# Kernel tuning notes

Measured on AMD Instinct MI355X. Metric: run time of the kernel, lower is better.

## Reference

```python
import jax, jax.numpy as jnp
import numpy as np

NUM_LAYER = 3
LEAKY = 0.8
RES = 0.8  # residual scale in convolution


def spmm(row, col, val, x, n):
    # sparse (n x n) COO @ dense (n x d)
    return jax.ops.segment_sum(val[:, None] * x[col], row, num_segments=n)


def convolution(emb, row, col, val):
    n = emb.shape[0]
    all_e = emb
    acc = emb  # layer-0 term
    for _ in range(NUM_LAYER):
        all_e = spmm(row, col, val, all_e, n) + RES * all_e
        acc = acc + all_e
    return acc / (NUM_LAYER + 1)


def setup_inputs() -> dict:
    key = jax.random.key(0)
    ks = jax.random.split(key, 32)
    B, NU, NQ, NC, DE, DF = 16384, 50000, 20000, 512, 64, 128
    EU, EQ, EK = 1600000, 640000, 16384
    inp = {}
    inp['user_id'] = jax.random.randint(ks[0], (B,), 0, NU)
    inp['question_id'] = jax.random.randint(ks[1], (B,), 0, NQ)
    inp['q_table'] = (jax.random.uniform(ks[2], (NQ, NC)) < 0.05).astype(jnp.float32)
    inp['u_row'] = jax.random.randint(ks[3], (EU,), 0, NU)
    inp['u_col'] = jax.random.randint(ks[4], (EU,), 0, NU)
    inp['u_val'] = jax.random.uniform(ks[5], (EU,)) / 32.0
    inp['e_row'] = jax.random.randint(ks[6], (EQ,), 0, NQ)
    inp['e_col'] = jax.random.randint(ks[7], (EQ,), 0, NQ)
    inp['e_val'] = jax.random.uniform(ks[8], (EQ,)) / 32.0
    inp['k_row'] = jax.random.randint(ks[9], (EK,), 0, NC)
    inp['k_col'] = jax.random.randint(ks[10], (EK,), 0, NC)
    inp['k_val'] = jax.random.uniform(ks[11], (EK,)) / 32.0
    inp['student_emb'] = jax.random.normal(ks[12], (NU, DE)) * 0.1
    inp['exercise_emb'] = jax.random.normal(ks[13], (NQ, DE)) * 0.1
    inp['knowledge_emb'] = jax.random.normal(ks[14], (NC, DE)) * 0.1
    inp['W_s'] = jax.random.normal(ks[15], (DE, DF)) * 0.1
    inp['b_s'] = jnp.zeros((DF,))
    inp['W_e'] = jax.random.normal(ks[16], (DE, DF)) * 0.1
    inp['b_e'] = jnp.zeros((DF,))
    inp['W_k'] = jax.random.normal(ks[17], (DE, DF)) * 0.1
    inp['b_k'] = jnp.zeros((DF,))
    inp['W_d'] = jax.random.normal(ks[18], (DE, 1)) * 0.1
    inp['b_d'] = jnp.zeros((1,))
    inp['M1_w'] = jax.random.normal(ks[19], (NC, 512)) * 0.05
    inp['M1_b'] = jnp.zeros((512,))
    inp['M2_w'] = jax.random.normal(ks[20], (512, 256)) * 0.05
    inp['M2_b'] = jnp.zeros((256,))
    inp['M3_w'] = jax.random.normal(ks[21], (256, 128)) * 0.05
    inp['M3_b'] = jnp.zeros((128,))
    inp['M4_w'] = jax.random.normal(ks[22], (128, 1)) * 0.05
    inp['M4_b'] = jnp.zeros((1,))
    return inp


def reference(user_id, question_id, q_table,
              u_row, u_col, u_val, e_row, e_col, e_val, k_row, k_col, k_val,
              student_emb, exercise_emb, knowledge_emb,
              W_s, b_s, W_e, b_e, W_k, b_k, W_d, b_d,
              M1_w, M1_b, M2_w, M2_b, M3_w, M3_b, M4_w, M4_b):
    cs = convolution(student_emb, u_row, u_col, u_val)    # [NU, DE]
    ce = convolution(exercise_emb, e_row, e_col, e_val)   # [NQ, DE]
    ck = convolution(knowledge_emb, k_row, k_col, k_val)  # [NC, DE]
    bs = cs[user_id]        # [B, DE]
    be = ce[question_id]    # [B, DE]
    sf = jax.nn.leaky_relu(bs @ W_s + b_s, LEAKY)   # [B, DF]
    ef = jax.nn.leaky_relu(be @ W_e + b_e, LEAKY)   # [B, DF]
    kf = jax.nn.leaky_relu(ck @ W_k + b_k, LEAKY)   # [NC, DF]
    disc = jax.nn.sigmoid(be @ W_d + b_d)           # [B, 1]
    state = disc * ((sf - ef) @ kf.T) * q_table[question_id]  # [B, NC]
    h = jnp.tanh(state @ M1_w + M1_b)
    h = jnp.tanh(h @ M2_w + M2_b)
    h = jnp.tanh(h @ M3_w + M3_b)
    return jax.nn.sigmoid(h @ M4_w + M4_b).reshape(-1)  # [B]
```

## Files before the change

kernel.cpp:

```cpp
#include <hip/hip_runtime.h>
#include <hip/hip_bf16.h>
#include <math.h>

#define RESF 0.8f
#define LEAKYF 0.8f
#define BWSH 6
#define BWID 64
#define BSTRIDE 2432

typedef __attribute__((ext_vector_type(8))) short bs8;
typedef __attribute__((ext_vector_type(4))) float f32x4;

__device__ __forceinline__ void gload16(const void* g, void* l) {
  __builtin_amdgcn_global_load_lds((const __attribute__((address_space(1))) void*)g,
                                   (__attribute__((address_space(3))) void*)l, 16, 0, 0);
}

__device__ __forceinline__ float tanh_fast(float x) {
  float t = __expf(2.f * x);
  return 1.f - 2.f * __builtin_amdgcn_rcpf(1.f + t);
}
__device__ __forceinline__ float sigmoid_fast(float x) {
  return __builtin_amdgcn_rcpf(1.f + __expf(-x));
}
__device__ __forceinline__ ushort f2bf(float a) {
  __hip_bfloat16 h = __float2bfloat16(a);
  return *(ushort*)&h;
}

__device__ __forceinline__ void edge_full(int e,
    const int* __restrict__ rU, const int* __restrict__ cU, const float* __restrict__ vU,
    const int* __restrict__ rE, const int* __restrict__ cE, const float* __restrict__ vE,
    const int* __restrict__ rK, const int* __restrict__ cK, const float* __restrict__ vK,
    int EU, int EQ, int NU, int NQ, int& grow, int& gcol, float& val) {
  if (e < EU) { grow = rU[e]; gcol = cU[e]; val = vU[e]; return; }
  if ((e -= EU) < EQ) { grow = NU + rE[e]; gcol = NU + cE[e]; val = vE[e]; return; }
  e -= EQ;
  grow = NU + NQ + rK[e]; gcol = NU + NQ + cK[e]; val = vK[e];
}

__global__ __launch_bounds__(256) void k_setup(int* __restrict__ gcur, int* __restrict__ flags,
                                               int nbuck, int N_tot) {
  int i = blockIdx.x * 256 + threadIdx.x;
  if (i < nbuck) gcur[i] = 0;
  if (i < N_tot) flags[i] = 0;
}

template <int BINR>
__global__ __launch_bounds__(1024) void k_bin(
    const int* __restrict__ rU, const int* __restrict__ cU, const float* __restrict__ vU,
    const int* __restrict__ rE, const int* __restrict__ cE, const float* __restrict__ vE,
    const int* __restrict__ rK, const int* __restrict__ cK, const float* __restrict__ vK,
    int* __restrict__ gcur, int2* __restrict__ tmp,
    int EU, int EQ, int EK, int NU, int NQ, int nbuck) {
  const int BINCH = BINR * 1024;
  extern __shared__ int l[];
  int metaN = (2 * nbuck + 3) & ~3;
  int* cnt = l;
  int* dstb = l + nbuck;
  int2* spk = (int2*)(l + metaN);
  ushort* sbk = (ushort*)(spk + BINCH);
  __shared__ int wsum[16];

  int t = threadIdx.x;
  int lane = t & 63, wid = t >> 6;
  for (int i = t; i < nbuck; i += 1024) cnt[i] = 0;
  __syncthreads();

  int E = EU + EQ + EK;
  int lo = blockIdx.x * BINCH;
  int hi = lo + BINCH < E ? lo + BINCH : E;
  int m = hi - lo;

  int2 pk[BINR];
  int bk[BINR];
#pragma unroll
  for (int k = 0; k < BINR; ++k) {
    int e = lo + t + k * 1024;
    bk[k] = -1;
    if (e < hi) {
      int grow, gcol;
      float val;
      edge_full(e, rU, cU, vU, rE, cE, vE, rK, cK, vK, EU, EQ, NU, NQ, grow, gcol, val);
      pk[k].x = ((grow & (BWID - 1)) << 26) | gcol;
      pk[k].y = __float_as_int(val);
      int b = grow >> BWSH;
      bk[k] = b;
      atomicAdd(&cnt[b], 1);
    }
  }
  __syncthreads();

  int carry = 0;
  for (int base = 0; base < nbuck; base += 1024) {
    int i = base + t;
    int x = (i < nbuck) ? cnt[i] : 0;
    int v = x;
#pragma unroll
    for (int d = 1; d < 64; d <<= 1) {
      int y = __shfl_up(v, d);
      if (lane >= d) v += y;
    }
    if (lane == 63) wsum[wid] = v;
    __syncthreads();
    if (t < 16) {
      int w = wsum[t];
#pragma unroll
      for (int d = 1; d < 16; d <<= 1) {
        int y = __shfl_up(w, d);
        if (t >= d) w += y;
      }
      wsum[t] = w;
    }
    __syncthreads();
    int excl = carry + ((wid > 0) ? wsum[wid - 1] : 0) + v - x;
    if (i < nbuck) {
      int gb = x ? atomicAdd(&gcur[i], x) : 0;
      dstb[i] = (i * BSTRIDE + gb) - excl;
      cnt[i] = excl;
    }
    carry += wsum[15];
    __syncthreads();
  }

#pragma unroll
  for (int k = 0; k < BINR; ++k) {
    if (bk[k] >= 0) {
      int p = atomicAdd(&cnt[bk[k]], 1);
      spk[p] = pk[k];
      sbk[p] = (ushort)bk[k];
    }
  }
  __syncthreads();

  for (int i = t; i < m; i += 1024) {
    int b = sbk[i];
    tmp[dstb[b] + i] = spk[i];
  }
}

__global__ __launch_bounds__(256) void k_sort(const int2* __restrict__ tmp, int2* __restrict__ sorted,
                                              const int* __restrict__ gcur,
                                              int* __restrict__ roff2, int N_tot) {
  __shared__ int2 sedge[BSTRIDE];
  __shared__ int cnt[BWID];
  __shared__ int cur[BWID];
  int b = blockIdx.x, t = threadIdx.x;
  int beg = b * BSTRIDE;
  int cb = gcur[b];
  int m = cb < BSTRIDE ? cb : BSTRIDE;
  if (t < BWID) cnt[t] = 0;
  __syncthreads();
  for (int i = t; i < m; i += 256) {
    int2 pe = tmp[beg + i];
    sedge[i] = pe;
    atomicAdd(&cnt[((unsigned)pe.x) >> 26], 1);
  }
  __syncthreads();
  if (t < BWID) {
    int x = cnt[t];
    int v = x;
#pragma unroll
    for (int d = 1; d < 64; d <<= 1) {
      int y = __shfl_up(v, d);
      if (t >= d) v += y;
    }
    cur[t] = v - x;
    roff2[b * (BWID + 1) + t] = beg + v - x;
  } else if (t == BWID) {
    roff2[b * (BWID + 1) + BWID] = beg + m;
  }
  __syncthreads();
  for (int i = t; i < m; i += 256) {
    int2 pe = sedge[i];
    int rl = ((unsigned)pe.x) >> 26;
    int rank = atomicAdd(&cur[rl], 1);
    sorted[beg + rank] = pe;
  }
}

__global__ __launch_bounds__(256) void k_initflag(ushort* __restrict__ lay0,
                                                  const float* __restrict__ embU,
                                                  const float* __restrict__ embE,
                                                  const float* __restrict__ embK,
                                                  int n4U, int n4E, int n4K,
                                                  const int* __restrict__ user_id,
                                                  const int* __restrict__ question_id,
                                                  int* __restrict__ flags,
                                                  int B, int NU, int NUQ, int NC) {
  int gid = blockIdx.x * 256 + threadIdx.x;
  if (gid < B) {
    flags[user_id[gid]] = 1;
    flags[NU + question_id[gid]] = 1;
  }
  if (gid < NC) flags[NUQ + gid] = 1;

  int n4 = n4U + n4E + n4K;
  int stride = gridDim.x * 256;
  ushort4* c4 = (ushort4*)lay0;
  for (int i = gid; i < n4; i += stride) {
    const float4* src;
    int j = i;
    if (j < n4U) src = (const float4*)embU;
    else if ((j -= n4U) < n4E) src = (const float4*)embE;
    else { j -= n4E; src = (const float4*)embK; }
    float4 v = src[j];
    ushort4 u;
    u.x = f2bf(v.x); u.y = f2bf(v.y); u.z = f2bf(v.z); u.w = f2bf(v.w);
    c4[i] = u;
  }
}

__device__ __forceinline__ void spmm_core(const ushort* __restrict__ curb,
                                          const int2* __restrict__ edges,
                                          int beg, int end, int li, int eh,
                                          float& a0, float& a1, float& a2, float& a3) {
  int lane = (eh << 4) | li;
  for (int base = beg; base < end; base += 64) {
    int rem = end - base;
    int m = rem < 64 ? rem : 64;
    int c = 0, vi = 0;
    if (lane < m) {
      int2 pe = edges[base + lane];
      c = pe.x & 0x3FFFFFF;
      vi = pe.y;
    }
    for (int j = 0; j * 4 < m; j += 8) {
      int cc[8];
      float vf[8];
#pragma unroll
      for (int k = 0; k < 8; ++k) {
        int s = (j + k) * 4 + eh;
        cc[k] = __shfl(c, s);
        vf[k] = __int_as_float(__shfl(vi, s));
      }
      uint2 x[8];
#pragma unroll
      for (int k = 0; k < 8; ++k)
        x[k] = *(const uint2*)&curb[(size_t)cc[k] * 64 + 4 * li];
#pragma unroll
      for (int k = 0; k < 8; ++k) {
        a0 = fmaf(vf[k], __uint_as_float(x[k].x << 16), a0);
        a1 = fmaf(vf[k], __uint_as_float(x[k].x & 0xffff0000u), a1);
        a2 = fmaf(vf[k], __uint_as_float(x[k].y << 16), a2);
        a3 = fmaf(vf[k], __uint_as_float(x[k].y & 0xffff0000u), a3);
      }
    }
  }
  a0 += __shfl_xor(a0, 16); a0 += __shfl_xor(a0, 32);
  a1 += __shfl_xor(a1, 16); a1 += __shfl_xor(a1, 32);
  a2 += __shfl_xor(a2, 16); a2 += __shfl_xor(a2, 32);
  a3 += __shfl_xor(a3, 16); a3 += __shfl_xor(a3, 32);
}

__global__ __launch_bounds__(256) void k_spmm2(const ushort* __restrict__ curb,
                                               ushort* __restrict__ nxtb,
                                               const int* __restrict__ roff2,
                                               const int2* __restrict__ edges, int n) {
  int r = blockIdx.x * 4 + (threadIdx.x >> 6);
  if (r >= n) return;
  int ro = (r >> BWSH) * (BWID + 1) + (r & (BWID - 1));
  int lane = threadIdx.x & 63;
  int li = lane & 15, eh = lane >> 4;
  int beg = roff2[ro], end = roff2[ro + 1];
  float a0 = 0.f, a1 = 0.f, a2 = 0.f, a3 = 0.f;
  spmm_core(curb, edges, beg, end, li, eh, a0, a1, a2, a3);
  if (eh == 0) {
    size_t gi = (size_t)r * 64 + 4 * li;
    uint2 cv = *(const uint2*)&curb[gi];
    a0 = fmaf(RESF, __uint_as_float(cv.x << 16), a0);
    a1 = fmaf(RESF, __uint_as_float(cv.x & 0xffff0000u), a1);
    a2 = fmaf(RESF, __uint_as_float(cv.y << 16), a2);
    a3 = fmaf(RESF, __uint_as_float(cv.y & 0xffff0000u), a3);
    uint2 o;
    o.x = ((unsigned)f2bf(a1) << 16) | f2bf(a0);
    o.y = ((unsigned)f2bf(a3) << 16) | f2bf(a2);
    *(uint2*)&nxtb[gi] = o;
  }
}

__global__ __launch_bounds__(256) void k_spmm3(const ushort* __restrict__ curb,
                                               const ushort* __restrict__ lay1,
                                               const float* __restrict__ embU,
                                               const float* __restrict__ embE,
                                               const float* __restrict__ embK,
                                               float* __restrict__ acc,
                                               const int* __restrict__ roff2,
                                               const int2* __restrict__ edges,
                                               const int* __restrict__ flags,
                                               int NU, int NQ, int n) {
  int r = blockIdx.x * 4 + (threadIdx.x >> 6);
  if (r >= n) return;
  if (!flags[r]) return;
  int ro = (r >> BWSH) * (BWID + 1) + (r & (BWID - 1));
  int lane = threadIdx.x & 63;
  int li = lane & 15, eh = lane >> 4;
  int beg = roff2[ro], end = roff2[ro + 1];
  float a0 = 0.f, a1 = 0.f, a2 = 0.f, a3 = 0.f;
  spmm_core(curb, edges, beg, end, li, eh, a0, a1, a2, a3);
  if (eh == 0) {
    size_t gi = (size_t)r * 64 + 4 * li;
    const float* ep;
    if (r < NU) ep = embU + gi;
    else if (r < NU + NQ) ep = embE + (gi - (size_t)NU * 64);
    else ep = embK + (gi - (size_t)(NU + NQ) * 64);
    float4 e = *(const float4*)ep;
    uint2 l1 = *(const uint2*)&lay1[gi];
    uint2 c2 = *(const uint2*)&curb[gi];
    float c20 = __uint_as_float(c2.x << 16);
    float c21 = __uint_as_float(c2.x & 0xffff0000u);
    float c22 = __uint_as_float(c2.y << 16);
    float c23 = __uint_as_float(c2.y & 0xffff0000u);
    float4 o;
    o.x = e.x + __uint_as_float(l1.x << 16) + c20 + fmaf(RESF, c20, a0);
    o.y = e.y + __uint_as_float(l1.x & 0xffff0000u) + c21 + fmaf(RESF, c21, a1);
    o.z = e.z + __uint_as_float(l1.y << 16) + c22 + fmaf(RESF, c22, a2);
    o.w = e.w + __uint_as_float(l1.y & 0xffff0000u) + c23 + fmaf(RESF, c23, a3);
    *(float4*)&acc[gi] = o;
  }
}

__global__ __launch_bounds__(256) void k_prep(const float* __restrict__ acc_k,
                                              const float* __restrict__ W_k, const float* __restrict__ b_k,
                                              __hip_bfloat16* __restrict__ kfb,
                                              const float* __restrict__ M1_w, __hip_bfloat16* __restrict__ W1t,
                                              const float* __restrict__ M2_w, __hip_bfloat16* __restrict__ W2t,
                                              const float* __restrict__ M3_w, __hip_bfloat16* __restrict__ W3t) {
  int idx = blockIdx.x * 256 + threadIdx.x;
  if (idx < 65536) {
    int d = idx & 127, c = idx >> 7;
    float a = b_k[d];
#pragma unroll 8
    for (int k = 0; k < 64; ++k) a += 0.25f * acc_k[c * 64 + k] * W_k[k * 128 + d];
    float v = a > 0.f ? a : LEAKYF * a;
    kfb[c * 128 + d] = __float2bfloat16(v);
    return;
  }
  int j = idx - 65536;
  if (j < 262144) {
    int n = j >> 9, k = j & 511;
    W1t[n * 512 + k] = __float2bfloat16(M1_w[k * 512 + n]);
    return;
  }
  j -= 262144;
  if (j < 131072) {
    int n = j >> 9, k = j & 511;
    W2t[n * 512 + k] = __float2bfloat16(M2_w[k * 256 + n]);
    return;
  }
  j -= 131072;
  if (j < 32768) {
    int n = j >> 8, k = j & 255;
    W3t[n * 256 + k] = __float2bfloat16(M3_w[k * 128 + n]);
  }
}

__global__ __launch_bounds__(256) void k_diff(
    const int* __restrict__ user_id, const int* __restrict__ question_id,
    const float* __restrict__ acc_u, const float* __restrict__ acc_e,
    const float* __restrict__ W_s, const float* __restrict__ b_s,
    const float* __restrict__ W_e, const float* __restrict__ b_e,
    const float* __restrict__ W_d, const float* __restrict__ b_d,
    __hip_bfloat16* __restrict__ diff, float* __restrict__ disc, int B) {
  __shared__ float bs_l[16 * 64];
  __shared__ float be_l[16 * 64];
  int t = threadIdx.x;
  int row0 = blockIdx.x * 16;
  for (int i = t; i < 16 * 64; i += 256) {
    int r = i >> 6, d = i & 63;
    int gb = row0 + r;
    bs_l[i] = 0.25f * acc_u[(size_t)user_id[gb] * 64 + d];
    be_l[i] = 0.25f * acc_e[(size_t)question_id[gb] * 64 + d];
  }
  __syncthreads();

  int j = t & 127, half = t >> 7;
  float as[8], ae[8];
#pragma unroll
  for (int rr = 0; rr < 8; ++rr) { as[rr] = b_s[j]; ae[rr] = b_e[j]; }
#pragma unroll 4
  for (int k = 0; k < 64; ++k) {
    float ws = W_s[k * 128 + j];
    float we = W_e[k * 128 + j];
#pragma unroll
    for (int rr = 0; rr < 8; ++rr) {
      as[rr] = fmaf(bs_l[(half * 8 + rr) * 64 + k], ws, as[rr]);
      ae[rr] = fmaf(be_l[(half * 8 + rr) * 64 + k], we, ae[rr]);
    }
  }
#pragma unroll
  for (int rr = 0; rr < 8; ++rr) {
    float sfv = as[rr] > 0.f ? as[rr] : LEAKYF * as[rr];
    float efv = ae[rr] > 0.f ? ae[rr] : LEAKYF * ae[rr];
    diff[(size_t)(row0 + half * 8 + rr) * 128 + j] = __float2bfloat16(sfv - efv);
  }
  if (t < 16) {
    float a = b_d[0];
#pragma unroll 8
    for (int k = 0; k < 64; ++k) a = fmaf(be_l[t * 64 + k], W_d[k], a);
    disc[row0 + t] = sigmoid_fast(a);
  }
}

template <int K, int MODE>
__global__ __launch_bounds__(256) void k_gemm(
    const __hip_bfloat16* __restrict__ A, const __hip_bfloat16* __restrict__ Bw,
    __hip_bfloat16* __restrict__ C, int N,
    const float* __restrict__ bias,
    const float* __restrict__ disc, const int* __restrict__ qid,
    const float* __restrict__ q_table,
    const float* __restrict__ M4w, const float* __restrict__ M4b,
    float* __restrict__ outp) {
  __shared__ __align__(16) short lA[128 * 32];
  __shared__ __align__(16) short lB[128 * 32];
  __shared__ float s_disc[128];
  __shared__ int s_qid[128];
  __shared__ float s_bias[128];
  __shared__ float sM4[128];
  __shared__ float spart[128][2];

  int t = threadIdx.x;
  int lane = t & 63;
  int w = t >> 6;
  int wr = (w >> 1) * 64, wc = (w & 1) * 64;
  int bm0 = blockIdx.y * 128, bn0 = blockIdx.x * 128;

  if (MODE == 0) {
    if (t < 128) {
      s_disc[t] = disc[bm0 + t];
      s_qid[t] = qid[bm0 + t];
    }
  } else {
    if (t < 128) s_bias[t] = bias[bn0 + t];
    if (MODE == 2 && t < 128) sM4[t] = M4w[t];
  }

  int off0 = t, off1 = 256 + t;
  int rA0 = off0 >> 2, gq0 = (off0 & 3) ^ ((rA0 >> 1) & 3);
  int rA1 = off1 >> 2, gq1 = (off1 & 3) ^ ((rA1 >> 1) & 3);

  const __hip_bfloat16* Ab = A + (size_t)bm0 * K;
  const __hip_bfloat16* Bb = Bw + (size_t)bn0 * K;

  f32x4 acc[4][4] = {};
  int q = lane >> 4, fr = lane & 15;

  for (int k0 = 0; k0 < K; k0 += 32) {
    __syncthreads();
    gload16(Ab + (size_t)rA0 * K + k0 + gq0 * 8, lA + (size_t)off0 * 8);
    gload16(Ab + (size_t)rA1 * K + k0 + gq1 * 8, lA + (size_t)off1 * 8);
    gload16(Bb + (size_t)rA0 * K + k0 + gq0 * 8, lB + (size_t)off0 * 8);
    gload16(Bb + (size_t)rA1 * K + k0 + gq1 * 8, lB + (size_t)off1 * 8);
    __syncthreads();

    bs8 af[4], bf[4];
#pragma unroll
    for (int mi = 0; mi < 4; ++mi) {
      int row = wr + mi * 16 + fr;
      int a16 = row * 4 + (q ^ ((row >> 1) & 3));
      af[mi] = *(const bs8*)&lA[a16 * 8];
    }
#pragma unroll
    for (int ni = 0; ni < 4; ++ni) {
      int col = wc + ni * 16 + fr;
      int b16 = col * 4 + (q ^ ((col >> 1) & 3));
      bf[ni] = *(const bs8*)&lB[b16 * 8];
    }
#pragma unroll
    for (int mi = 0; mi < 4; ++mi)
#pragma unroll
      for (int ni = 0; ni < 4; ++ni)
        acc[mi][ni] = __builtin_amdgcn_mfma_f32_16x16x32_bf16(af[mi], bf[ni], acc[mi][ni], 0, 0, 0);
  }

  if (MODE == 2) {
#pragma unroll
    for (int mi = 0; mi < 4; ++mi) {
#pragma unroll
      for (int j = 0; j < 4; ++j) {
        int lr = wr + mi * 16 + q * 4 + j;
        float p = 0.f;
#pragma unroll
        for (int ni = 0; ni < 4; ++ni) {
          int lc = wc + ni * 16 + fr;
          p += tanh_fast(acc[mi][ni][j] + s_bias[lc]) * sM4[lc];
        }
        p += __shfl_xor(p, 1);
        p += __shfl_xor(p, 2);
        p += __shfl_xor(p, 4);
        p += __shfl_xor(p, 8);
        if (fr == 0) spart[lr][w & 1] = p;
      }
    }
    __syncthreads();
    if (t < 128) outp[bm0 + t] = sigmoid_fast(spart[t][0] + spart[t][1] + M4b[0]);
    return;
  }

#pragma unroll
  for (int mi = 0; mi < 4; ++mi) {
    int lr0 = wr + mi * 16 + q * 4;
#pragma unroll
    for (int j = 0; j < 4; ++j) {
      int lr = lr0 + j;
      size_t gr = bm0 + lr;
      float dsc = 0.f;
      size_t qrow = 0;
      if (MODE == 0) {
        dsc = s_disc[lr];
        qrow = (size_t)s_qid[lr] * 512;
      }
#pragma unroll
      for (int ni = 0; ni < 4; ++ni) {
        int lc = wc + ni * 16 + fr;
        int gc = bn0 + lc;
        float v = acc[mi][ni][j];
        if (MODE == 0) {
          v = dsc * v * q_table[qrow + gc];
        } else {
          v = tanh_fast(v + s_bias[lc]);
        }
        C[gr * N + gc] = __float2bfloat16(v);
      }
    }
  }
}

static inline int iminh(int a, int b) { return a < b ? a : b; }
static inline size_t rnd4(size_t x) { return (x + 3) & ~(size_t)3; }

extern "C" void kernel_launch(void* const* d_in, const int* in_sizes, int n_in,
                              void* d_out, int out_size, void* d_ws, size_t ws_size,
                              hipStream_t stream) {
  const int* user_id = (const int*)d_in[0];
  const int* question_id = (const int*)d_in[1];
  const float* q_table = (const float*)d_in[2];
  const int* u_row = (const int*)d_in[3];
  const int* u_col = (const int*)d_in[4];
  const float* u_val = (const float*)d_in[5];
  const int* e_row = (const int*)d_in[6];
  const int* e_col = (const int*)d_in[7];
  const float* e_val = (const float*)d_in[8];
  const int* k_row = (const int*)d_in[9];
  const int* k_col = (const int*)d_in[10];
  const float* k_val = (const float*)d_in[11];
  const float* student_emb = (const float*)d_in[12];
  const float* exercise_emb = (const float*)d_in[13];
  const float* knowledge_emb = (const float*)d_in[14];
  const float* W_s = (const float*)d_in[15];
  const float* b_s = (const float*)d_in[16];
  const float* W_e = (const float*)d_in[17];
  const float* b_e = (const float*)d_in[18];
  const float* W_k = (const float*)d_in[19];
  const float* b_k = (const float*)d_in[20];
  const float* W_d = (const float*)d_in[21];
  const float* b_d = (const float*)d_in[22];
  const float* M1_w = (const float*)d_in[23];
  const float* M1_b = (const float*)d_in[24];
  const float* M2_w = (const float*)d_in[25];
  const float* M2_b = (const float*)d_in[26];
  const float* M3_w = (const float*)d_in[27];
  const float* M3_b = (const float*)d_in[28];
  const float* M4_w = (const float*)d_in[29];
  const float* M4_b = (const float*)d_in[30];

  int B = in_sizes[0];
  int NU = in_sizes[12] / 64;
  int NQ = in_sizes[13] / 64;
  int NC = in_sizes[14] / 64;
  int EU = in_sizes[3];
  int EQ = in_sizes[6];
  int EK = in_sizes[9];
  int N_tot = NU + NQ + NC;
  int E_tot = EU + EQ + EK;
  int nbuck = (N_tot + BWID - 1) >> BWSH;

  float* w = (float*)d_ws;
  float* acc = w; w += rnd4((size_t)N_tot * 64);
  __hip_bfloat16* kfb = (__hip_bfloat16*)w; w += rnd4(512 * 128 / 2);
  float* U = w;

  float* acc_u = acc;
  float* acc_e = acc + (size_t)NU * 64;
  float* acc_k = acc + (size_t)(NU + NQ) * 64;

  float* cw = U;
  ushort* lay0 = (ushort*)cw; cw += rnd4((size_t)N_tot * 32);
  ushort* lay1 = (ushort*)cw; cw += rnd4((size_t)N_tot * 32);
  int2* sorted = (int2*)cw;   cw += rnd4((size_t)nbuck * BSTRIDE * 2);
  int* gcur = (int*)cw;  cw += rnd4(nbuck);
  int* flags = (int*)cw; cw += rnd4(N_tot);
  int* roff2 = (int*)cw; cw += rnd4((size_t)nbuck * (BWID + 1) + 4);
  float* alias0 = cw;
  int2* tmp = (int2*)alias0;
  ushort* lay2 = (ushort*)alias0;
  {
    size_t tmp_f = rnd4((size_t)nbuck * BSTRIDE * 2);
    size_t lay_f = rnd4((size_t)N_tot * 32);
    cw += (tmp_f > lay_f ? tmp_f : lay_f);
  }

  float* mw = U;
  __hip_bfloat16* W1t = (__hip_bfloat16*)mw; mw += rnd4(512 * 512 / 2);
  __hip_bfloat16* W2t = (__hip_bfloat16*)mw; mw += rnd4(256 * 512 / 2);
  __hip_bfloat16* W3t = (__hip_bfloat16*)mw; mw += rnd4(128 * 256 / 2);
  __hip_bfloat16* diff = (__hip_bfloat16*)mw; mw += rnd4((size_t)B * 128 / 2);
  float* disc = mw; mw += rnd4(B);
  __hip_bfloat16* state = (__hip_bfloat16*)mw; mw += rnd4((size_t)B * 512 / 2);
  __hip_bfloat16* h1 = (__hip_bfloat16*)mw;    mw += rnd4((size_t)B * 512 / 2);
  __hip_bfloat16* h2 = state;

  static int big_ok = -1;
  if (big_ok < 0) {
    hipError_t e = hipFuncSetAttribute((const void*)k_bin<10>,
                                       hipFuncAttributeMaxDynamicSharedMemorySize,
                                       160 * 1024);
    big_ok = (e == hipSuccess) ? 1 : 0;
    (void)hipGetLastError();
  }

  {
    int metaN = (2 * nbuck + 3) & ~3;
    k_setup<<<(N_tot + 255) / 256, 256, 0, stream>>>(gcur, flags, nbuck, N_tot);
    if (big_ok) {
      const int BINCH = 10240;
      int gsb = (E_tot + BINCH - 1) / BINCH;
      size_t ldsb = (size_t)metaN * 4 + (size_t)BINCH * 8 + (size_t)BINCH * 2;
      k_bin<10><<<gsb, 1024, ldsb, stream>>>(u_row, u_col, u_val, e_row, e_col, e_val,
                                             k_row, k_col, k_val, gcur, tmp,
                                             EU, EQ, EK, NU, NQ, nbuck);
    } else {
      const int BINCH = 5120;
      int gsb = (E_tot + BINCH - 1) / BINCH;
      size_t ldsb = (size_t)metaN * 4 + (size_t)BINCH * 8 + (size_t)BINCH * 2;
      k_bin<5><<<gsb, 1024, ldsb, stream>>>(u_row, u_col, u_val, e_row, e_col, e_val,
                                            k_row, k_col, k_val, gcur, tmp,
                                            EU, EQ, EK, NU, NQ, nbuck);
    }
    k_sort<<<nbuck, 256, 0, stream>>>(tmp, sorted, gcur, roff2, N_tot);
  }

  {
    int n4 = N_tot * 16;
    int gs = iminh((n4 + 255) / 256, 2048);
    k_initflag<<<gs, 256, 0, stream>>>(lay0, student_emb, exercise_emb, knowledge_emb,
                                       NU * 16, NQ * 16, NC * 16,
                                       user_id, question_id, flags, B, NU, NU + NQ, NC);
    k_spmm2<<<(N_tot + 3) / 4, 256, 0, stream>>>(lay0, lay1, roff2, sorted, N_tot);
    k_spmm2<<<(N_tot + 3) / 4, 256, 0, stream>>>(lay1, lay2, roff2, sorted, N_tot);
    k_spmm3<<<(N_tot + 3) / 4, 256, 0, stream>>>(lay2, lay1, student_emb, exercise_emb,
                                                 knowledge_emb, acc, roff2, sorted,
                                                 flags, NU, NQ, N_tot);
  }

  k_prep<<<(65536 + 262144 + 131072 + 32768) / 256, 256, 0, stream>>>(
      acc_k, W_k, b_k, kfb, M1_w, W1t, M2_w, W2t, M3_w, W3t);

  k_diff<<<B / 16, 256, 0, stream>>>(user_id, question_id, acc_u, acc_e,
                                     W_s, b_s, W_e, b_e, W_d, b_d, diff, disc, B);

  k_gemm<128, 0><<<dim3(512 / 128, B / 128), 256, 0, stream>>>(
      diff, kfb, state, 512, nullptr, disc, question_id, q_table, nullptr, nullptr, nullptr);
  k_gemm<512, 1><<<dim3(512 / 128, B / 128), 256, 0, stream>>>(
      state, W1t, h1, 512, M1_b, nullptr, nullptr, nullptr, nullptr, nullptr, nullptr);
  k_gemm<512, 1><<<dim3(256 / 128, B / 128), 256, 0, stream>>>(
      h1, W2t, h2, 256, M2_b, nullptr, nullptr, nullptr, nullptr, nullptr, nullptr);
  k_gemm<256, 2><<<dim3(1, B / 128), 256, 0, stream>>>(
      h2, W3t, nullptr, 128, M3_b, nullptr, nullptr, nullptr, M4_w, M4_b, (float*)d_out);
}
```

Measured before the change: 223.4 us.

## Make SpMM kernels persistent with software-prefetched row offsets and edges

```diff
diff --git a/kernel.cpp b/kernel.cpp
--- a/kernel.cpp
+++ b/kernel.cpp
@@ -7,6 +7,7 @@
 #define BWSH 6
 #define BWID 64
 #define BSTRIDE 2432
+#define SPMMNB 2048
 
 typedef __attribute__((ext_vector_type(8))) short bs8;
 typedef __attribute__((ext_vector_type(4))) float f32x4;
@@ -211,41 +212,50 @@
   }
 }
 
-__device__ __forceinline__ void spmm_core(const ushort* __restrict__ curb,
-                                          const int2* __restrict__ edges,
-                                          int beg, int end, int li, int eh,
-                                          float& a0, float& a1, float& a2, float& a3) {
-  int lane = (eh << 4) | li;
-  for (int base = beg; base < end; base += 64) {
+__device__ __forceinline__ void spmm_window(const ushort* __restrict__ curb,
+                                            int c, int vi, int m, int li, int eh,
+                                            float& a0, float& a1, float& a2, float& a3) {
+  for (int j = 0; j * 4 < m; j += 8) {
+    int cc[8];
+    float vf[8];
+#pragma unroll
+    for (int k = 0; k < 8; ++k) {
+      int s = (j + k) * 4 + eh;
+      cc[k] = __shfl(c, s);
+      vf[k] = __int_as_float(__shfl(vi, s));
+    }
+    uint2 x[8];
+#pragma unroll
+    for (int k = 0; k < 8; ++k)
+      x[k] = *(const uint2*)&curb[(size_t)cc[k] * 64 + 4 * li];
+#pragma unroll
+    for (int k = 0; k < 8; ++k) {
+      a0 = fmaf(vf[k], __uint_as_float(x[k].x << 16), a0);
+      a1 = fmaf(vf[k], __uint_as_float(x[k].x & 0xffff0000u), a1);
+      a2 = fmaf(vf[k], __uint_as_float(x[k].y << 16), a2);
+      a3 = fmaf(vf[k], __uint_as_float(x[k].y & 0xffff0000u), a3);
+    }
+  }
+}
+
+__device__ __forceinline__ void spmm_row(const ushort* __restrict__ curb,
+                                         const int2* __restrict__ edges,
+                                         int beg, int end, int c, int vi,
+                                         int lane, int li, int eh,
+                                         float& a0, float& a1, float& a2, float& a3) {
+  int m0 = end - beg;
+  m0 = m0 < 64 ? m0 : 64;
+  spmm_window(curb, c, vi, m0, li, eh, a0, a1, a2, a3);
+  for (int base = beg + 64; base < end; base += 64) {
     int rem = end - base;
     int m = rem < 64 ? rem : 64;
-    int c = 0, vi = 0;
+    int cc = 0, vv = 0;
     if (lane < m) {
       int2 pe = edges[base + lane];
-      c = pe.x & 0x3FFFFFF;
-      vi = pe.y;
-    }
-    for (int j = 0; j * 4 < m; j += 8) {
-      int cc[8];
-      float vf[8];
-#pragma unroll
-      for (int k = 0; k < 8; ++k) {
-        int s = (j + k) * 4 + eh;
-        cc[k] = __shfl(c, s);
-        vf[k] = __int_as_float(__shfl(vi, s));
-      }
-      uint2 x[8];
-#pragma unroll
-      for (int k = 0; k < 8; ++k)
-        x[k] = *(const uint2*)&curb[(size_t)cc[k] * 64 + 4 * li];
-#pragma unroll
-      for (int k = 0; k < 8; ++k) {
-        a0 = fmaf(vf[k], __uint_as_float(x[k].x << 16), a0);
-        a1 = fmaf(vf[k], __uint_as_float(x[k].x & 0xffff0000u), a1);
-        a2 = fmaf(vf[k], __uint_as_float(x[k].y << 16), a2);
-        a3 = fmaf(vf[k], __uint_as_float(x[k].y & 0xffff0000u), a3);
-      }
-    }
+      cc = pe.x & 0x3FFFFFF;
+      vv = pe.y;
+    }
+    spmm_window(curb, cc, vv, m, li, eh, a0, a1, a2, a3);
   }
   a0 += __shfl_xor(a0, 16); a0 += __shfl_xor(a0, 32);
   a1 += __shfl_xor(a1, 16); a1 += __shfl_xor(a1, 32);
@@ -253,29 +263,61 @@
   a3 += __shfl_xor(a3, 16); a3 += __shfl_xor(a3, 32);
 }
 
+__device__ __forceinline__ int ro_of(int r) {
+  return (r >> BWSH) * (BWID + 1) + (r & (BWID - 1));
+}
+
 __global__ __launch_bounds__(256) void k_spmm2(const ushort* __restrict__ curb,
                                                ushort* __restrict__ nxtb,
                                                const int* __restrict__ roff2,
                                                const int2* __restrict__ edges, int n) {
-  int r = blockIdx.x * 4 + (threadIdx.x >> 6);
-  if (r >= n) return;
-  int ro = (r >> BWSH) * (BWID + 1) + (r & (BWID - 1));
+  int nw = gridDim.x * 4;
+  int wv = blockIdx.x * 4 + (threadIdx.x >> 6);
   int lane = threadIdx.x & 63;
   int li = lane & 15, eh = lane >> 4;
+
+  int r = wv;
+  if (r >= n) return;
+  int ro = ro_of(r);
   int beg = roff2[ro], end = roff2[ro + 1];
-  float a0 = 0.f, a1 = 0.f, a2 = 0.f, a3 = 0.f;
-  spmm_core(curb, edges, beg, end, li, eh, a0, a1, a2, a3);
-  if (eh == 0) {
-    size_t gi = (size_t)r * 64 + 4 * li;
-    uint2 cv = *(const uint2*)&curb[gi];
-    a0 = fmaf(RESF, __uint_as_float(cv.x << 16), a0);
-    a1 = fmaf(RESF, __uint_as_float(cv.x & 0xffff0000u), a1);
-    a2 = fmaf(RESF, __uint_as_float(cv.y << 16), a2);
-    a3 = fmaf(RESF, __uint_as_float(cv.y & 0xffff0000u), a3);
-    uint2 o;
-    o.x = ((unsigned)f2bf(a1) << 16) | f2bf(a0);
-    o.y = ((unsigned)f2bf(a3) << 16) | f2bf(a2);
-    *(uint2*)&nxtb[gi] = o;
+  int r1 = r + nw, beg1 = 0, end1 = 0;
+  if (r1 < n) {
+    int ro1 = ro_of(r1);
+    beg1 = roff2[ro1]; end1 = roff2[ro1 + 1];
+  }
+  int c = 0, vi = 0;
+  {
+    int m = end - beg; m = m < 64 ? m : 64;
+    if (lane < m) { int2 pe = edges[beg + lane]; c = pe.x & 0x3FFFFFF; vi = pe.y; }
+  }
+  while (true) {
+    int r2 = r1 + nw, beg2 = 0, end2 = 0;
+    if (r2 < n) {
+      int ro2 = ro_of(r2);
+      beg2 = roff2[ro2]; end2 = roff2[ro2 + 1];
+    }
+    int c1 = 0, vi1 = 0;
+    if (r1 < n) {
+      int m = end1 - beg1; m = m < 64 ? m : 64;
+      if (lane < m) { int2 pe = edges[beg1 + lane]; c1 = pe.x & 0x3FFFFFF; vi1 = pe.y; }
+    }
+    float a0 = 0.f, a1 = 0.f, a2 = 0.f, a3 = 0.f;
+    spmm_row(curb, edges, beg, end, c, vi, lane, li, eh, a0, a1, a2, a3);
+    if (eh == 0) {
+      size_t gi = (size_t)r * 64 + 4 * li;
+      uint2 cv = *(const uint2*)&curb[gi];
+      a0 = fmaf(RESF, __uint_as_float(cv.x << 16), a0);
+      a1 = fmaf(RESF, __uint_as_float(cv.x & 0xffff0000u), a1);
+      a2 = fmaf(RESF, __uint_as_float(cv.y << 16), a2);
+      a3 = fmaf(RESF, __uint_as_float(cv.y & 0xffff0000u), a3);
+      uint2 o;
+      o.x = ((unsigned)f2bf(a1) << 16) | f2bf(a0);
+      o.y = ((unsigned)f2bf(a3) << 16) | f2bf(a2);
+      *(uint2*)&nxtb[gi] = o;
+    }
+    if (r1 >= n) break;
+    r = r1; beg = beg1; end = end1; c = c1; vi = vi1;
+    r1 = r2; beg1 = beg2; end1 = end2;
   }
 }
 
@@ -289,34 +331,66 @@
                                                const int2* __restrict__ edges,
                                                const int* __restrict__ flags,
                                                int NU, int NQ, int n) {
-  int r = blockIdx.x * 4 + (threadIdx.x >> 6);
-  if (r >= n) return;
-  if (!flags[r]) return;
-  int ro = (r >> BWSH) * (BWID + 1) + (r & (BWID - 1));
+  int nw = gridDim.x * 4;
+  int wv = blockIdx.x * 4 + (threadIdx.x >> 6);
   int lane = threadIdx.x & 63;
   int li = lane & 15, eh = lane >> 4;
+
+  int r = wv;
+  if (r >= n) return;
+  int fl = flags[r];
+  int ro = ro_of(r);
   int beg = roff2[ro], end = roff2[ro + 1];
-  float a0 = 0.f, a1 = 0.f, a2 = 0.f, a3 = 0.f;
-  spmm_core(curb, edges, beg, end, li, eh, a0, a1, a2, a3);
-  if (eh == 0) {
-    size_t gi = (size_t)r * 64 + 4 * li;
-    const float* ep;
-    if (r < NU) ep = embU + gi;
-    else if (r < NU + NQ) ep = embE + (gi - (size_t)NU * 64);
-    else ep = embK + (gi - (size_t)(NU + NQ) * 64);
-    float4 e = *(const float4*)ep;
-    uint2 l1 = *(const uint2*)&lay1[gi];
-    uint2 c2 = *(const uint2*)&curb[gi];
-    float c20 = __uint_as_float(c2.x << 16);
-    float c21 = __uint_as_float(c2.x & 0xffff0000u);
-    float c22 = __uint_as_float(c2.y << 16);
-    float c23 = __uint_as_float(c2.y & 0xffff0000u);
-    float4 o;
-    o.x = e.x + __uint_as_float(l1.x << 16) + c20 + fmaf(RESF, c20, a0);
-    o.y = e.y + __uint_as_float(l1.x & 0xffff0000u) + c21 + fmaf(RESF, c21, a1);
-    o.z = e.z + __uint_as_float(l1.y << 16) + c22 + fmaf(RESF, c22, a2);
-    o.w = e.w + __uint_as_float(l1.y & 0xffff0000u) + c23 + fmaf(RESF, c23, a3);
-    *(float4*)&acc[gi] = o;
+  int r1 = r + nw, fl1 = 0, beg1 = 0, end1 = 0;
+  if (r1 < n) {
+    fl1 = flags[r1];
+    int ro1 = ro_of(r1);
+    beg1 = roff2[ro1]; end1 = roff2[ro1 + 1];
+  }
+  int c = 0, vi = 0;
+  if (fl) {
+    int m = end - beg; m = m < 64 ? m : 64;
+    if (lane < m) { int2 pe = edges[beg + lane]; c = pe.x & 0x3FFFFFF; vi = pe.y; }
+  }
+  while (true) {
+    int r2 = r1 + nw, fl2 = 0, beg2 = 0, end2 = 0;
+    if (r2 < n) {
+      fl2 = flags[r2];
+      int ro2 = ro_of(r2);
+      beg2 = roff2[ro2]; end2 = roff2[ro2 + 1];
+    }
+    int c1 = 0, vi1 = 0;
+    if (fl1) {
+      int m = end1 - beg1; m = m < 64 ? m : 64;
+      if (lane < m) { int2 pe = edges[beg1 + lane]; c1 = pe.x & 0x3FFFFFF; vi1 = pe.y; }
+    }
+    if (fl) {
+      float a0 = 0.f, a1 = 0.f, a2 = 0.f, a3 = 0.f;
+      spmm_row(curb, edges, beg, end, c, vi, lane, li, eh, a0, a1, a2, a3);
+      if (eh == 0) {
+        size_t gi = (size_t)r * 64 + 4 * li;
+        const float* ep;
+        if (r < NU) ep = embU + gi;
+        else if (r < NU + NQ) ep = embE + (gi - (size_t)NU * 64);
+        else ep = embK + (gi - (size_t)(NU + NQ) * 64);
+        float4 e = *(const float4*)ep;
+        uint2 l1 = *(const uint2*)&lay1[gi];
+        uint2 c2 = *(const uint2*)&curb[gi];
+        float c20 = __uint_as_float(c2.x << 16);
+        float c21 = __uint_as_float(c2.x & 0xffff0000u);
+        float c22 = __uint_as_float(c2.y << 16);
+        float c23 = __uint_as_float(c2.y & 0xffff0000u);
+        float4 o;
+        o.x = e.x + __uint_as_float(l1.x << 16) + c20 + fmaf(RESF, c20, a0);
+        o.y = e.y + __uint_as_float(l1.x & 0xffff0000u) + c21 + fmaf(RESF, c21, a1);
+        o.z = e.z + __uint_as_float(l1.y << 16) + c22 + fmaf(RESF, c22, a2);
+        o.w = e.w + __uint_as_float(l1.y & 0xffff0000u) + c23 + fmaf(RESF, c23, a3);
+        *(float4*)&acc[gi] = o;
+      }
+    }
+    if (r1 >= n) break;
+    r = r1; fl = fl1; beg = beg1; end = end1; c = c1; vi = vi1;
+    r1 = r2; fl1 = fl2; beg1 = beg2; end1 = end2;
   }
 }
 
@@ -646,11 +720,11 @@
     k_initflag<<<gs, 256, 0, stream>>>(lay0, student_emb, exercise_emb, knowledge_emb,
                                        NU * 16, NQ * 16, NC * 16,
                                        user_id, question_id, flags, B, NU, NU + NQ, NC);
-    k_spmm2<<<(N_tot + 3) / 4, 256, 0, stream>>>(lay0, lay1, roff2, sorted, N_tot);
-    k_spmm2<<<(N_tot + 3) / 4, 256, 0, stream>>>(lay1, lay2, roff2, sorted, N_tot);
-    k_spmm3<<<(N_tot + 3) / 4, 256, 0, stream>>>(lay2, lay1, student_emb, exercise_emb,
-                                                 knowledge_emb, acc, roff2, sorted,
-                                                 flags, NU, NQ, N_tot);
+    k_spmm2<<<SPMMNB, 256, 0, stream>>>(lay0, lay1, roff2, sorted, N_tot);
+    k_spmm2<<<SPMMNB, 256, 0, stream>>>(lay1, lay2, roff2, sorted, N_tot);
+    k_spmm3<<<SPMMNB, 256, 0, stream>>>(lay2, lay1, student_emb, exercise_emb,
+                                        knowledge_emb, acc, roff2, sorted,
+                                        flags, NU, NQ, N_tot);
   }
 
   k_prep<<<(65536 + 262144 + 131072 + 32768) / 256, 256, 0, stream>>>(
```

New measurement: 245.2 us. 9.8% more time.
